# Kernel optimization log

Measured on AMD Instinct MI355X. Metric: run time of the kernel, lower is better.

## Reference

```python
import jax, jax.numpy as jnp
import numpy as np

MODES = 20
WIDTH = 64
EPS = 1e-5


def spectral_conv(x, w1, w2, m1, m2):
    # x: [B, C, H, W] real; w1, w2: [Ci, Co, m1, m2, 2] (real/imag)
    B, C, H, W = x.shape
    xf = jnp.fft.rfft2(x, norm='ortho')  # [B, C, H, W//2+1] complex
    w1c = w1[..., 0] + 1j * w1[..., 1]
    w2c = w2[..., 0] + 1j * w2[..., 1]
    m1 = min(m1, H)
    m2 = min(m2, W // 2 + 1)
    top = jnp.einsum('bixy,ioxy->boxy', xf[:, :, :m1, :m2], w1c[:, :, :m1, :m2])
    bot = jnp.einsum('bixy,ioxy->boxy', xf[:, :, -m1:, :m2], w2c[:, :, :m1, :m2])
    out = jnp.zeros((B, w1.shape[1], H, W // 2 + 1), dtype=xf.dtype)
    out = out.at[:, :, :m1, :m2].set(top)
    out = out.at[:, :, H - m1:, :m2].set(bot)
    return jnp.fft.irfft2(out, s=(H, W), norm='ortho')


def batchnorm2d(x, gamma, beta):
    # training-mode BN over (B, H, W) per channel; x: [B, C, H, W]
    mean = jnp.mean(x, axis=(0, 2, 3), keepdims=True)
    var = jnp.var(x, axis=(0, 2, 3), keepdims=True)
    xn = (x - mean) * jax.lax.rsqrt(var + EPS)
    return xn * gamma[None, :, None, None] + beta[None, :, None, None]


def setup_inputs() -> dict:
    key = jax.random.key(0)
    ks = jax.random.split(key, 12)
    B, H, W, Tin2 = 8, 256, 256, 12
    scale = 1.0 / (WIDTH * WIDTH)
    return {
        'x': jax.random.normal(ks[0], (B, H, W, Tin2), jnp.float32),
        'fc0_w': jax.random.normal(ks[1], (Tin2, WIDTH), jnp.float32) * 0.1,
        'fc0_b': jnp.zeros((WIDTH,), jnp.float32),
        'sw1': scale * jax.random.normal(ks[2], (4, WIDTH, WIDTH, MODES, MODES, 2), jnp.float32),
        'sw2': scale * jax.random.normal(ks[3], (4, WIDTH, WIDTH, MODES, MODES, 2), jnp.float32),
        'cw': jax.random.normal(ks[4], (4, WIDTH, WIDTH), jnp.float32) * 0.1,
        'cb': jnp.zeros((4, WIDTH), jnp.float32),
        'bng': jnp.ones((4, WIDTH), jnp.float32),
        'bnb': jnp.zeros((4, WIDTH), jnp.float32),
        'fc1_w': jax.random.normal(ks[5], (WIDTH, 128), jnp.float32) * 0.1,
        'fc1_b': jnp.zeros((128,), jnp.float32),
        'fc2_w': jax.random.normal(ks[6], (128, 1), jnp.float32) * 0.1,
        'fc2_b': jnp.zeros((1,), jnp.float32),
    }


def reference(x, fc0_w, fc0_b, sw1, sw2, cw, cb, bng, bnb, fc1_w, fc1_b, fc2_w, fc2_b):
    # lift: [B, H, W, Tin+2] -> [B, C, H, W]
    h = jnp.einsum('bhwt,tc->bhwc', x, fc0_w) + fc0_b
    h = jnp.transpose(h, (0, 3, 1, 2))
    for l in range(4):
        spec = spectral_conv(h, sw1[l], sw2[l], MODES, MODES)
        lin = jnp.einsum('bihw,oi->bohw', h, cw[l]) + cb[l][None, :, None, None]
        h = batchnorm2d(spec + lin, bng[l], bnb[l])
        if l < 3:
            h = jax.nn.relu(h)
    h = jnp.transpose(h, (0, 2, 3, 1))  # [B, H, W, C]
    h = jax.nn.relu(jnp.einsum('bhwc,cd->bhwd', h, fc1_w) + fc1_b)
    out = jnp.einsum('bhwd,de->bhwe', h, fc2_w) + fc2_b
    return out
```

## Files before the change

### kernel.cpp

```cpp
#include <hip/hip_runtime.h>
#include <hip/hip_bf16.h>


__device__ __forceinline__ void gll16(const float* gsrc, float* ldst) {
    __builtin_amdgcn_global_load_lds(
        (const __attribute__((address_space(1))) void*)gsrc,
        (__attribute__((address_space(3))) void*)ldst, 16, 0, 0);
}

__device__ __forceinline__ unsigned bfp(float x) {
    unsigned u = __float_as_uint(x);
    return (u + 0x7fffu + ((u >> 16) & 1u)) >> 16;
}

#define UNPK(U, B4) \
    B4.x = __uint_as_float((U).x << 16); B4.y = __uint_as_float((U).x & 0xffff0000u); \
    B4.z = __uint_as_float((U).y << 16); B4.w = __uint_as_float((U).y & 0xffff0000u);

__global__ __launch_bounds__(256) void init_k(const float* __restrict__ cw,
                                              float* __restrict__ costab, float* __restrict__ sintab,
                                              float* __restrict__ EAt, float* __restrict__ Tw,
                                              float* __restrict__ cwT, float* __restrict__ stats,
                                              unsigned* __restrict__ Twh) {
    int idx = blockIdx.x * 256 + threadIdx.x;
    const float PH = 6.28318530717958647692f / 256.f;
    if (idx < 256) {
        float s, c; sincosf(idx * PH, &s, &c);
        costab[idx] = c; sintab[idx] = s;
    } else if (idx < 256 + 10240) {
        int e = idx - 256;
        int n = e >> 8, w = e & 255, ky = n >> 1;
        int r = (ky * w) & 255;
        float s, c; sincosf(r * PH, &s, &c);
        EAt[e] = (n & 1) ? -s : c;
    } else if (idx < 256 + 20480) {
        int e = idx - 10496;
        int kp = e >> 8, w = e & 255;
        int ky = kp >> 1, p = kp & 1;
        int r = (ky * w) & 255;
        float s, c; sincosf(r * PH, &s, &c);
        float v;
        if (ky == 0) v = p ? 0.f : (1.f / 16.f);
        else         v = p ? (-2.f / 16.f) * s : (2.f / 16.f) * c;
        Tw[e] = v;
    } else if (idx < 256 + 20480 + 16384) {
        int e = idx - 20736;
        int l = e >> 12, r2 = e & 4095;
        int i = r2 >> 6, o = r2 & 63;
        cwT[e] = cw[(l << 12) + (o << 6) + i];
    } else if (idx < 256 + 20480 + 16384 + 2048) {
        stats[idx - 37120] = 0.f;
    } else if (idx < 256 + 20480 + 16384 + 2048 + 5120) {
        int e = idx - 39168;
        int kp = e >> 7, w2 = e & 127;
        int ky = kp >> 1, p = kp & 1;
        float v0, v1;
        {
            int w = w2 << 1;
            int r = (ky * w) & 255;
            float s, c; sincosf(r * PH, &s, &c);
            v0 = (ky == 0) ? (p ? 0.f : (1.f / 16.f))
                           : (p ? (-2.f / 16.f) * s : (2.f / 16.f) * c);
            r = (ky * (w + 1)) & 255;
            sincosf(r * PH, &s, &c);
            v1 = (ky == 0) ? (p ? 0.f : (1.f / 16.f))
                           : (p ? (-2.f / 16.f) * s : (2.f / 16.f) * c);
        }
        Twh[e] = bfp(v0) | (bfp(v1) << 16);
    }
}

__global__ __launch_bounds__(256) void wtrans_k(const float* __restrict__ sw1,
                                                const float* __restrict__ sw2,
                                                unsigned int* __restrict__ wt) {
    int gid = blockIdx.x * 4 + (threadIdx.x >> 6);
    int o = threadIdx.x & 63;
    int xyc = gid % 25;
    int i = (gid / 25) & 63;
    int t2 = gid / 1600;
    const float* src = ((t2 & 1) ? sw2 : sw1) + (t2 >> 1) * 3276800;
    const float* sp = src + ((i * 64 + o) * 400 + xyc * 16) * 2;
    unsigned int* dp = wt + (size_t)(t2 * 400 + xyc * 16) * 4096 + i * 64 + o;
#pragma unroll
    for (int j = 0; j < 16; ++j) {
        float re = sp[2 * j], im = sp[2 * j + 1];
        dp[(size_t)j * 4096] = bfp(re) | (bfp(im) << 16);
    }
}

__global__ __launch_bounds__(256) void fc0_k(const float* __restrict__ x,
                                             const float* __restrict__ w,
                                             const float* __restrict__ bias,
                                             float* __restrict__ outb) {
    __shared__ float ws[768];
    __shared__ float bs[64];
    int tid = threadIdx.x;
    for (int i = tid; i < 768; i += 256) ws[i] = w[i];
    if (tid < 64) bs[tid] = bias[tid];
    __syncthreads();
    int pix = blockIdx.x * 256 + tid;
    int b = pix >> 16, hw = pix & 65535;
    float xv[12];
#pragma unroll
    for (int t = 0; t < 12; ++t) xv[t] = x[pix * 12 + t];
    int base = (b << 22) + hw;
    for (int c = 0; c < 64; ++c) {
        float a = bs[c];
#pragma unroll
        for (int t = 0; t < 12; ++t) a += xv[t] * ws[t * 64 + c];
        outb[base + (c << 16)] = a;
    }
}

__global__ __launch_bounds__(128) void dftw_k(const float* __restrict__ X,
                                              const float* __restrict__ EAt,
                                              float* __restrict__ T,
                                              const float* __restrict__ statsl,
                                              const float* __restrict__ g,
                                              const float* __restrict__ bt,
                                              int fuse) {
    __shared__ __align__(16) float Xs[32 * 68];
    __shared__ __align__(16) float Est[40 * 32];
    int tid = threadIdx.x;
    int tm = tid >> 3, tn = tid & 7;
    int row0 = blockIdx.x << 6;
    float sc = 1.f, sh = 0.f;
    if (fuse) {
        int c = (row0 >> 8) & 63;
        float ssum = statsl[c] + statsl[128 + c] + statsl[256 + c] + statsl[384 + c];
        float ssq  = statsl[64 + c] + statsl[192 + c] + statsl[320 + c] + statsl[448 + c];
        float mean = ssum * (1.f / 524288.f);
        float var = ssq * (1.f / 524288.f) - mean * mean;
        sc = g[c] * rsqrtf(var + 1e-5f);
        sh = bt[c] - mean * sc;
    }
    float acc[4][5];
#pragma unroll
    for (int i = 0; i < 4; ++i)
#pragma unroll
        for (int j = 0; j < 5; ++j) acc[i][j] = 0.f;

#pragma unroll 1
    for (int kc = 0; kc < 256; kc += 32) {
        __syncthreads();
#pragma unroll
        for (int r = 0; r < 4; ++r) {
            int m = tm + (r << 4);
            float4 v = *(const float4*)&X[(row0 + m) * 256 + kc + (tn << 2)];
            if (fuse) {
                v.x = fmaxf(fmaf(v.x, sc, sh), 0.f);
                v.y = fmaxf(fmaf(v.y, sc, sh), 0.f);
                v.z = fmaxf(fmaf(v.z, sc, sh), 0.f);
                v.w = fmaxf(fmaf(v.w, sc, sh), 0.f);
            }
            int kb = tn << 2;
            Xs[(kb + 0) * 68 + m] = v.x;
            Xs[(kb + 1) * 68 + m] = v.y;
            Xs[(kb + 2) * 68 + m] = v.z;
            Xs[(kb + 3) * 68 + m] = v.w;
        }
        for (int i = tid; i < 1280; i += 128) Est[i] = EAt[((i >> 5) << 8) + kc + (i & 31)];
        __syncthreads();
#pragma unroll 1
        for (int k4 = 0; k4 < 8; ++k4) {
            float4 e0 = *(const float4*)&Est[(tn * 5 + 0) * 32 + (k4 << 2)];
            float4 e1 = *(const float4*)&Est[(tn * 5 + 1) * 32 + (k4 << 2)];
            float4 e2 = *(const float4*)&Est[(tn * 5 + 2) * 32 + (k4 << 2)];
            float4 e3 = *(const float4*)&Est[(tn * 5 + 3) * 32 + (k4 << 2)];
            float4 e4 = *(const float4*)&Est[(tn * 5 + 4) * 32 + (k4 << 2)];
#pragma unroll
            for (int c2 = 0; c2 < 4; ++c2) {
                float4 a = *(const float4*)&Xs[((k4 << 2) + c2) * 68 + (tm << 2)];
                float ev0 = ((const float*)&e0)[c2];
                float ev1 = ((const float*)&e1)[c2];
                float ev2 = ((const float*)&e2)[c2];
                float ev3 = ((const float*)&e3)[c2];
                float ev4 = ((const float*)&e4)[c2];
                acc[0][0] += a.x * ev0; acc[1][0] += a.y * ev0; acc[2][0] += a.z * ev0; acc[3][0] += a.w * ev0;
                acc[0][1] += a.x * ev1; acc[1][1] += a.y * ev1; acc[2][1] += a.z * ev1; acc[3][1] += a.w * ev1;
                acc[0][2] += a.x * ev2; acc[1][2] += a.y * ev2; acc[2][2] += a.z * ev2; acc[3][2] += a.w * ev2;
                acc[0][3] += a.x * ev3; acc[1][3] += a.y * ev3; acc[2][3] += a.z * ev3; acc[3][3] += a.w * ev3;
                acc[0][4] += a.x * ev4; acc[1][4] += a.y * ev4; acc[2][4] += a.z * ev4; acc[3][4] += a.w * ev4;
            }
        }
    }
#pragma unroll
    for (int i = 0; i < 4; ++i) {
        int row = row0 + (tm << 2) + i;
#pragma unroll
        for (int j = 0; j < 5; ++j) T[row * 40 + tn * 5 + j] = acc[i][j];
    }
}

__global__ __launch_bounds__(256) void dfth_k(const float* __restrict__ T,
                                              const float* __restrict__ ct, const float* __restrict__ st,
                                              float* __restrict__ XF) {
    __shared__ __align__(16) float Ts[10240];
    __shared__ float cts[256], sts[256];
    int tid = threadIdx.x;
    int bc = blockIdx.x;
    for (int i = tid; i < 10240; i += 256) Ts[i] = T[bc * 10240 + i];
    cts[tid] = ct[tid]; sts[tid] = st[tid];
    __syncthreads();
    if (tid < 200) {
        int kxi = tid / 5, kyg = tid % 5;
        int kxa = kxi < 20 ? kxi : kxi + 216;
        float ar0 = 0, ai0 = 0, ar1 = 0, ai1 = 0, ar2 = 0, ai2 = 0, ar3 = 0, ai3 = 0;
        int r = 0;
#pragma unroll 1
        for (int h = 0; h < 256; ++h) {
            float cc = cts[r], sv = sts[r];
            r = (r + kxa) & 255;
            float4 v0 = *(const float4*)&Ts[h * 40 + (kyg << 3)];
            float4 v1 = *(const float4*)&Ts[h * 40 + (kyg << 3) + 4];
            ar0 += v0.x * cc + v0.y * sv;  ai0 += v0.y * cc - v0.x * sv;
            ar1 += v0.z * cc + v0.w * sv;  ai1 += v0.w * cc - v0.z * sv;
            ar2 += v1.x * cc + v1.y * sv;  ai2 += v1.y * cc - v1.x * sv;
            ar3 += v1.z * cc + v1.w * sv;  ai3 += v1.w * cc - v1.z * sv;
        }
        int b = bc >> 6, c = bc & 63;
        const float s = 1.f / 256.f;
        int A = (b * 40 + kxi) * 20 + (kyg << 2);
        float2* O = (float2*)XF;
        O[(A + 0) * 64 + c] = make_float2(ar0 * s, ai0 * s);
        O[(A + 1) * 64 + c] = make_float2(ar1 * s, ai1 * s);
        O[(A + 2) * 64 + c] = make_float2(ar2 * s, ai2 * s);
        O[(A + 3) * 64 + c] = make_float2(ar3 * s, ai3 * s);
    }
}

__global__ __launch_bounds__(512) void eins_t_k(const float* __restrict__ XF,
                                                const unsigned int* __restrict__ wtl,
                                                float* __restrict__ YF) {
    __shared__ float xfs[1024];
    int tid = threadIdx.x;
    int x = blockIdx.x / 20, y = blockIdx.x % 20;
    for (int i = tid; i < 1024; i += 512) {
        int b = i >> 7, rr = i & 127;
        xfs[i] = XF[(b * 40 + x) * 2560 + y * 128 + rr];
    }
    __syncthreads();
    int b = tid >> 6, o = tid & 63;
    const unsigned int* wp = wtl + (size_t)(((x < 20 ? 0 : 400) + (x % 20) * 20 + y)) * 4096 + o;
    float ar = 0.f, ai = 0.f;
#pragma unroll 8
    for (int i = 0; i < 64; ++i) {
        unsigned int wv = wp[i << 6];
        float wr = __uint_as_float(wv << 16);
        float wi = __uint_as_float(wv & 0xffff0000u);
        float xr = xfs[(b << 7) + (i << 1)];
        float xi = xfs[(b << 7) + (i << 1) + 1];
        ar += xr * wr - xi * wi;
        ai += xr * wi + xi * wr;
    }
    ((float2*)YF)[((b * 40 + x) * 20 + y) * 64 + o] = make_float2(ar, ai);
}

__global__ __launch_bounds__(512) void eins_k(const float* __restrict__ XF,
                                              const float* __restrict__ w1, const float* __restrict__ w2,
                                              float* __restrict__ YF) {
    __shared__ float xfs[1024];
    int tid = threadIdx.x;
    int x = blockIdx.x / 20, y = blockIdx.x % 20;
    for (int i = tid; i < 1024; i += 512) {
        int b = i >> 7, rr = i & 127;
        xfs[i] = XF[(b * 40 + x) * 2560 + y * 128 + rr];
    }
    __syncthreads();
    int b = tid >> 6, o = tid & 63;
    const float* wp = (x < 20) ? (w1 + (x * 20 + y) * 2) : (w2 + ((x - 20) * 20 + y) * 2);
    float ar = 0.f, ai = 0.f;
#pragma unroll 8
    for (int i = 0; i < 64; ++i) {
        float2 wv = *(const float2*)&wp[(i * 64 + o) * 800];
        float xr = xfs[(b << 7) + (i << 1)];
        float xi = xfs[(b << 7) + (i << 1) + 1];
        ar += xr * wv.x - xi * wv.y;
        ai += xr * wv.y + xi * wv.x;
    }
    ((float2*)YF)[((b * 40 + x) * 20 + y) * 64 + o] = make_float2(ar, ai);
}

__global__ __launch_bounds__(256) void idfth_k(const float* __restrict__ YF,
                                               const float* __restrict__ ct, const float* __restrict__ st,
                                               float* __restrict__ Z) {
    __shared__ __align__(16) float yfs[1600];
    __shared__ float cts[256], sts[256];
    int tid = threadIdx.x;
    int bc = blockIdx.x;
    int b = bc >> 6, co = bc & 63;
    for (int i = tid; i < 800; i += 256) {
        int kx = i / 20, ky = i % 20;
        float2 v = ((const float2*)YF)[((b * 40 + kx) * 20 + ky) * 64 + co];
        yfs[kx * 40 + 2 * ky] = v.x;
        yfs[kx * 40 + 2 * ky + 1] = v.y;
    }
    cts[tid] = ct[tid]; sts[tid] = st[tid];
    __syncthreads();
    int h = tid;
    float accr[20], acci[20];
#pragma unroll
    for (int q = 0; q < 20; ++q) { accr[q] = 0.f; acci[q] = 0.f; }
#pragma unroll 1
    for (int kxi = 0; kxi < 40; ++kxi) {
        int kxa = kxi < 20 ? kxi : kxi + 216;
        int r = (kxa * h) & 255;
        float cc = cts[r], sv = sts[r];
#pragma unroll
        for (int q = 0; q < 10; ++q) {
            float4 v = *(const float4*)&yfs[kxi * 40 + (q << 2)];
            accr[2 * q]     += v.x * cc - v.y * sv;  acci[2 * q]     += v.x * sv + v.y * cc;
            accr[2 * q + 1] += v.z * cc - v.w * sv;  acci[2 * q + 1] += v.z * sv + v.w * cc;
        }
    }
    const float s = 1.f / 16.f;
    int base = (bc * 256 + h) * 40;
#pragma unroll
    for (int q = 0; q < 10; ++q) {
        float4 o4;
        o4.x = accr[2 * q] * s;     o4.y = acci[2 * q] * s;
        o4.z = accr[2 * q + 1] * s; o4.w = acci[2 * q + 1] * s;
        *(float4*)&Z[base + (q << 2)] = o4;
    }
}

#define FMA2(I, AV, J, B4) \
    acc[I][J].x += (AV) * B4.x; acc[I][J].y += (AV) * B4.y; \
    acc[I][J].z += (AV) * B4.z; acc[I][J].w += (AV) * B4.w;

#define FMA_COL(J, B4) \
    FMA2(0, a0.x, J, B4) FMA2(1, a0.y, J, B4) FMA2(2, a0.z, J, B4) FMA2(3, a0.w, J, B4) \
    FMA2(4, a1.x, J, B4) FMA2(5, a1.y, J, B4) FMA2(6, a1.z, J, B4) FMA2(7, a1.w, J, B4)

__global__ __launch_bounds__(256) void speclin_k(const float* __restrict__ hin,
                                                 const float* __restrict__ Z,
                                                 const float* __restrict__ cwTl,
                                                 const unsigned* __restrict__ Twh,
                                                 const float* __restrict__ cbl,
                                                 float* __restrict__ pre,
                                                 float* __restrict__ statsl,
                                                 const float* __restrict__ statsp,
                                                 const float* __restrict__ gp,
                                                 const float* __restrict__ btp,
                                                 int fuse) {
    __shared__ __align__(16) float AZ[104 * 64];
    __shared__ __align__(16) unsigned short BsH[2][2048];
    __shared__ float scs[64], shs[64];
    int tid = threadIdx.x;
    int bh = blockIdx.x;
    int b = bh >> 8, h = bh & 255;
    int to = tid >> 5, tw = tid & 31;
    int o0 = to << 3;

    if (tid < 64) {
        float s = 1.f, so = 0.f;
        if (fuse) {
            float ssum = statsp[tid] + statsp[128 + tid] + statsp[256 + tid] + statsp[384 + tid];
            float ssq  = statsp[64 + tid] + statsp[192 + tid] + statsp[320 + tid] + statsp[448 + tid];
            float mean = ssum * (1.f / 524288.f);
            float var = ssq * (1.f / 524288.f) - mean * mean;
            s = gp[tid] * rsqrtf(var + 1e-5f);
            so = btp[tid] - mean * s;
        }
        scs[tid] = s; shs[tid] = so;
    }
#pragma unroll
    for (int t = 0; t < 4; ++t) {
        int i4 = tid + (t << 8);
        gll16(&cwTl[i4 << 2], &AZ[i4 << 2]);
    }
    {
        const float* Zrow = Z + ((size_t)(((b << 6) << 8) + h)) * 40;
#pragma unroll
        for (int t = 0; t < 3; ++t) {
            int i4 = tid + (t << 8);
            if (i4 < 640) {
                int q = i4 % 10, o = i4 / 10;
                float4 v = *(const float4*)&Zrow[o * 10240 + (q << 2)];
                int rb = ((64 + (q << 2)) << 6) + o;
                AZ[rb] = v.x; AZ[rb + 64] = v.y; AZ[rb + 128] = v.z; AZ[rb + 192] = v.w;
            }
        }
    }
    const float* hrow = hin + ((size_t)(((b << 6) << 8) + h) << 8);
    float4 st[2];
#pragma unroll
    for (int t = 0; t < 2; ++t) {
        int i4 = tid + (t << 8);
        st[t] = *(const float4*)&hrow[((i4 >> 6) << 16) + ((i4 & 63) << 2)];
    }
    __syncthreads();
#pragma unroll
    for (int t = 0; t < 2; ++t) {
        int i4 = tid + (t << 8);
        int k = i4 >> 6, w4 = i4 & 63;
        float4 v = st[t];
        if (fuse) {
            float sck = scs[k], shk = shs[k];
            v.x = fmaxf(fmaf(v.x, sck, shk), 0.f);
            v.y = fmaxf(fmaf(v.y, sck, shk), 0.f);
            v.z = fmaxf(fmaf(v.z, sck, shk), 0.f);
            v.w = fmaxf(fmaf(v.w, sck, shk), 0.f);
        }
        uint2 u = make_uint2(bfp(v.x) | (bfp(v.y) << 16), bfp(v.z) | (bfp(v.w) << 16));
        *(uint2*)&BsH[0][(k << 8) + (w4 << 2)] = u;
    }
    __syncthreads();

    float4 acc[8][2];
#pragma unroll
    for (int i = 0; i < 8; ++i) {
        acc[i][0] = make_float4(0.f, 0.f, 0.f, 0.f);
        acc[i][1] = make_float4(0.f, 0.f, 0.f, 0.f);
    }

    int cur = 0;
    uint2 stw[2];
#pragma unroll 1
    for (int ch = 0; ch < 8; ++ch) {
        if (ch < 7) {
#pragma unroll
            for (int t = 0; t < 2; ++t) {
                int i4 = tid + (t << 8);
                st[t] = *(const float4*)&hrow[((((ch + 1) << 3) + (i4 >> 6)) << 16) + ((i4 & 63) << 2)];
            }
        } else {
#pragma unroll
            for (int t = 0; t < 2; ++t)
                stw[t] = *(const uint2*)&Twh[(t << 9) + (tid << 1)];
        }
        const unsigned short* Bc = BsH[cur];
        const float* Ac = &AZ[((ch << 3) << 6) + o0];
#pragma unroll 2
        for (int kk = 0; kk < 8; ++kk) {
            float4 a0 = *(const float4*)&Ac[(kk << 6)];
            float4 a1 = *(const float4*)&Ac[(kk << 6) + 4];
            uint2 u0 = *(const uint2*)&Bc[(kk << 8) + (tw << 2)];
            uint2 u1 = *(const uint2*)&Bc[(kk << 8) + 128 + (tw << 2)];
            float4 b0, b1;
            UNPK(u0, b0)
            UNPK(u1, b1)
            FMA_COL(0, b0)
            FMA_COL(1, b1)
        }
        if (ch < 7) {
#pragma unroll
            for (int t = 0; t < 2; ++t) {
                int i4 = tid + (t << 8);
                int k = i4 >> 6, w4 = i4 & 63;
                float4 v = st[t];
                if (fuse) {
                    float sck = scs[((ch + 1) << 3) + k], shk = shs[((ch + 1) << 3) + k];
                    v.x = fmaxf(fmaf(v.x, sck, shk), 0.f);
                    v.y = fmaxf(fmaf(v.y, sck, shk), 0.f);
                    v.z = fmaxf(fmaf(v.z, sck, shk), 0.f);
                    v.w = fmaxf(fmaf(v.w, sck, shk), 0.f);
                }
                uint2 u = make_uint2(bfp(v.x) | (bfp(v.y) << 16), bfp(v.z) | (bfp(v.w) << 16));
                *(uint2*)&BsH[cur ^ 1][(k << 8) + (w4 << 2)] = u;
            }
        } else {
#pragma unroll
            for (int t = 0; t < 2; ++t)
                *(uint2*)&BsH[cur ^ 1][(((t << 9) + (tid << 1)) << 1)] = stw[t];
        }
        __syncthreads();
        cur ^= 1;
    }

#pragma unroll 1
    for (int ch = 0; ch < 5; ++ch) {
        if (ch < 4) {
#pragma unroll
            for (int t = 0; t < 2; ++t)
                stw[t] = *(const uint2*)&Twh[((ch + 1) << 10) + (t << 9) + (tid << 1)];
        }
        const unsigned short* Bc = BsH[cur];
        const float* Ac = &AZ[(((ch << 3) + 64) << 6) + o0];
#pragma unroll 2
        for (int kk = 0; kk < 8; ++kk) {
            float4 a0 = *(const float4*)&Ac[(kk << 6)];
            float4 a1 = *(const float4*)&Ac[(kk << 6) + 4];
            uint2 u0 = *(const uint2*)&Bc[(kk << 8) + (tw << 2)];
            uint2 u1 = *(const uint2*)&Bc[(kk << 8) + 128 + (tw << 2)];
            float4 b0, b1;
            UNPK(u0, b0)
            UNPK(u1, b1)
            FMA_COL(0, b0)
            FMA_COL(1, b1)
        }
        if (ch < 4) {
#pragma unroll
            for (int t = 0; t < 2; ++t)
                *(uint2*)&BsH[cur ^ 1][(((t << 9) + (tid << 1)) << 1)] = stw[t];
        }
        __syncthreads();
        cur ^= 1;
    }

    float* srep = statsl + ((bh & 3) << 7);
#pragma unroll
    for (int i = 0; i < 8; ++i) {
        float cbv = cbl[o0 + i];
        float sum = 0.f, sq = 0.f;
        size_t obase = ((size_t)((((b << 6) + o0 + i) << 8) + h) << 8);
#pragma unroll
        for (int j = 0; j < 2; ++j) {
            float4 v = acc[i][j];
            v.x += cbv; v.y += cbv; v.z += cbv; v.w += cbv;
            *(float4*)&pre[obase + (j << 7) + (tw << 2)] = v;
            sum += v.x + v.y + v.z + v.w;
            sq  += v.x * v.x + v.y * v.y + v.z * v.z + v.w * v.w;
        }
        sum += __shfl_xor(sum, 1);  sq += __shfl_xor(sq, 1);
        sum += __shfl_xor(sum, 2);  sq += __shfl_xor(sq, 2);
        sum += __shfl_xor(sum, 4);  sq += __shfl_xor(sq, 4);
        sum += __shfl_xor(sum, 8);  sq += __shfl_xor(sq, 8);
        sum += __shfl_xor(sum, 16); sq += __shfl_xor(sq, 16);
        if ((tid & 31) == 0) {
            atomicAdd(&srep[o0 + i], sum);
            atomicAdd(&srep[64 + o0 + i], sq);
        }
    }
}

__global__ __launch_bounds__(256, 2) void fc12_k(const float* __restrict__ hin,
                                                 const float* __restrict__ statsl,
                                                 const float* __restrict__ g,
                                                 const float* __restrict__ bt,
                                                 const float* __restrict__ w1, const float* __restrict__ b1,
                                                 const float* __restrict__ w2, const float* __restrict__ b2,
                                                 float* __restrict__ out) {
    __shared__ __align__(16) float As[64 * 128];
    __shared__ __align__(16) float Bs[2][2048];
    __shared__ float scs[64], shs[64], bias2[128];
    __shared__ __align__(16) float red[4 * 256];
    int tid = threadIdx.x;
    int bh = blockIdx.x;
    int b = bh >> 8, h = bh & 255;
    int to = tid >> 4, tw = tid & 15;
    int d0 = to << 3;

    if (tid < 64) {
        float ssum = statsl[tid] + statsl[128 + tid] + statsl[256 + tid] + statsl[384 + tid];
        float ssq  = statsl[64 + tid] + statsl[192 + tid] + statsl[320 + tid] + statsl[448 + tid];
        float mean = ssum * (1.f / 524288.f);
        float var = ssq * (1.f / 524288.f) - mean * mean;
        float s = g[tid] * rsqrtf(var + 1e-5f);
        scs[tid] = s; shs[tid] = bt[tid] - mean * s;
    }
    __syncthreads();
    for (int i = tid; i < 8192; i += 256) As[i] = w1[i] * scs[i >> 7];
    if (tid < 128) {
        float a = b1[tid];
        for (int c = 0; c < 64; ++c) a += shs[c] * w1[c * 128 + tid];
        bias2[tid] = a;
    }
    const float* hrow = hin + ((size_t)(((b << 6) << 8) + h) << 8);
#pragma unroll
    for (int t = 0; t < 2; ++t) {
        int i4 = tid + (t << 8);
        gll16(&hrow[((i4 >> 6) << 16) + ((i4 & 63) << 2)], &Bs[0][i4 << 2]);
    }
    __syncthreads();

    float4 acc[8][4];
#pragma unroll
    for (int i = 0; i < 8; ++i)
#pragma unroll
        for (int j = 0; j < 4; ++j) acc[i][j] = make_float4(0.f, 0.f, 0.f, 0.f);

    int cur = 0;
#pragma unroll 1
    for (int ch = 0; ch < 8; ++ch) {
        if (ch < 7) {
#pragma unroll
            for (int t = 0; t < 2; ++t) {
                int i4 = tid + (t << 8);
                int k = i4 >> 6, w4 = (i4 & 63) << 2;
                gll16(&hrow[((((ch + 1) << 3) + k) << 16) + w4], &Bs[cur ^ 1][i4 << 2]);
            }
        }
        const float* Bc = Bs[cur];
#pragma unroll 2
        for (int kk = 0; kk < 8; ++kk) {
            int gk = (ch << 3) + kk;
            float4 a0 = *(const float4*)&As[(gk << 7) + d0];
            float4 a1 = *(const float4*)&As[(gk << 7) + d0 + 4];
            float4 b0 = *(const float4*)&Bc[(kk << 8) + (tw << 2)];
            float4 b1 = *(const float4*)&Bc[(kk << 8) + 64 + (tw << 2)];
            FMA_COL(0, b0)
            FMA_COL(1, b1)
            float4 b2 = *(const float4*)&Bc[(kk << 8) + 128 + (tw << 2)];
            float4 b3 = *(const float4*)&Bc[(kk << 8) + 192 + (tw << 2)];
            FMA_COL(2, b2)
            FMA_COL(3, b3)
        }
        __syncthreads();
        cur ^= 1;
    }

    float bb[8], wv[8];
#pragma unroll
    for (int i = 0; i < 8; ++i) { bb[i] = bias2[d0 + i]; wv[i] = w2[d0 + i]; }
    float4 p[4];
#pragma unroll
    for (int j = 0; j < 4; ++j) {
        float4 v = make_float4(0.f, 0.f, 0.f, 0.f);
#pragma unroll
        for (int i = 0; i < 8; ++i) {
            v.x += fmaxf(acc[i][j].x + bb[i], 0.f) * wv[i];
            v.y += fmaxf(acc[i][j].y + bb[i], 0.f) * wv[i];
            v.z += fmaxf(acc[i][j].z + bb[i], 0.f) * wv[i];
            v.w += fmaxf(acc[i][j].w + bb[i], 0.f) * wv[i];
        }
        v.x += __shfl_xor(v.x, 16); v.y += __shfl_xor(v.y, 16);
        v.z += __shfl_xor(v.z, 16); v.w += __shfl_xor(v.w, 16);
        v.x += __shfl_xor(v.x, 32); v.y += __shfl_xor(v.y, 32);
        v.z += __shfl_xor(v.z, 32); v.w += __shfl_xor(v.w, 32);
        p[j] = v;
    }
    int wave = tid >> 6;
    if ((tid & 63) < 16) {
#pragma unroll
        for (int j = 0; j < 4; ++j)
            *(float4*)&red[(wave << 8) + (j << 6) + (tw << 2)] = p[j];
    }
    __syncthreads();
    float s2 = b2[0] + red[tid] + red[256 + tid] + red[512 + tid] + red[768 + tid];
    out[(b * 256 + h) * 256 + tid] = s2;
}

extern "C" void kernel_launch(void* const* d_in, const int* in_sizes, int n_in,
                              void* d_out, int out_size, void* d_ws, size_t ws_size,
                              hipStream_t stream) {
    (void)in_sizes; (void)n_in; (void)out_size;
    const float* x     = (const float*)d_in[0];
    const float* fc0_w = (const float*)d_in[1];
    const float* fc0_b = (const float*)d_in[2];
    const float* sw1   = (const float*)d_in[3];
    const float* sw2   = (const float*)d_in[4];
    const float* cw    = (const float*)d_in[5];
    const float* cb    = (const float*)d_in[6];
    const float* bng   = (const float*)d_in[7];
    const float* bnb   = (const float*)d_in[8];
    const float* fc1_w = (const float*)d_in[9];
    const float* fc1_b = (const float*)d_in[10];
    const float* fc2_w = (const float*)d_in[11];
    const float* fc2_b = (const float*)d_in[12];
    float* out = (float*)d_out;

    float* ws = (float*)d_ws;
    float* hbuf   = ws;
    float* tz     = hbuf + 33554432;
    float* xf     = tz + 5242880;
    float* yf     = xf + 819200;
    float* costab = yf + 819200;
    float* sintab = costab + 256;
    float* EAt    = sintab + 256;
    float* Tw     = EAt + 10240;
    float* cwT    = Tw + 10240;
    float* stats  = cwT + 16384;
    unsigned* Twh = (unsigned*)(stats + 2048);
    unsigned* wt  = Twh + 5120;

    size_t base_floats = 40473600 + 2048 + 5120;
    int use_wt = (ws_size >= (base_floats + 13107200ull) * 4ull) ? 1 : 0;

    init_k<<<173, 256, 0, stream>>>(cw, costab, sintab, EAt, Tw, cwT, stats, Twh);
    if (use_wt) wtrans_k<<<3200, 256, 0, stream>>>(sw1, sw2, wt);
    fc0_k<<<2048, 256, 0, stream>>>(x, fc0_w, fc0_b, hbuf);

    for (int l = 0; l < 4; ++l) {
        if (l == 0)
            dftw_k<<<2048, 128, 0, stream>>>(hbuf, EAt, tz, stats, bng, bnb, 0);
        else
            dftw_k<<<2048, 128, 0, stream>>>(hbuf, EAt, tz, stats + (l - 1) * 512,
                                             bng + (l - 1) * 64, bnb + (l - 1) * 64, 1);
        dfth_k<<<512, 256, 0, stream>>>(tz, costab, sintab, xf);
        if (use_wt)
            eins_t_k<<<800, 512, 0, stream>>>(xf, wt + (size_t)l * 2 * 400 * 4096, yf);
        else
            eins_k<<<800, 512, 0, stream>>>(xf, sw1 + l * 3276800, sw2 + l * 3276800, yf);
        idfth_k<<<512, 256, 0, stream>>>(yf, costab, sintab, tz);
        speclin_k<<<2048, 256, 0, stream>>>(hbuf, tz, cwT + l * 4096, Twh, cb + l * 64,
                                            hbuf, stats + l * 512,
                                            (l == 0) ? stats : stats + (l - 1) * 512,
                                            bng + (l ? (l - 1) * 64 : 0),
                                            bnb + (l ? (l - 1) * 64 : 0),
                                            l ? 1 : 0);
    }
    fc12_k<<<2048, 256, 0, stream>>>(hbuf, stats + 3 * 512, bng + 3 * 64, bnb + 3 * 64,
                                     fc1_w, fc1_b, fc2_w, fc2_b, out);
}
```

Baseline: 1.312 ms.

## Move speclin GEMM to bf16 MFMA with hi/lo split weights

Measured after the change: 1.799 ms. 37.1% more time.

```diff
diff --git a/kernel.cpp b/kernel.cpp
--- a/kernel.cpp
+++ b/kernel.cpp
@@ -1,6 +1,9 @@
 #include <hip/hip_runtime.h>
 #include <hip/hip_bf16.h>
 
+
+typedef __attribute__((ext_vector_type(8))) short bfrag;
+typedef __attribute__((ext_vector_type(4))) float f32x4;
 
 __device__ __forceinline__ void gll16(const float* gsrc, float* ldst) {
     __builtin_amdgcn_global_load_lds(
@@ -12,61 +15,50 @@
     unsigned u = __float_as_uint(x);
     return (u + 0x7fffu + ((u >> 16) & 1u)) >> 16;
 }
-
-#define UNPK(U, B4) \
-    B4.x = __uint_as_float((U).x << 16); B4.y = __uint_as_float((U).x & 0xffff0000u); \
-    B4.z = __uint_as_float((U).y << 16); B4.w = __uint_as_float((U).y & 0xffff0000u);
+__device__ __forceinline__ float ubf(unsigned h) { return __uint_as_float(h << 16); }
 
 __global__ __launch_bounds__(256) void init_k(const float* __restrict__ cw,
                                               float* __restrict__ costab, float* __restrict__ sintab,
-                                              float* __restrict__ EAt, float* __restrict__ Tw,
-                                              float* __restrict__ cwT, float* __restrict__ stats,
-                                              unsigned* __restrict__ Twh) {
+                                              float* __restrict__ EAt, float* __restrict__ stats,
+                                              unsigned* __restrict__ Twp, unsigned* __restrict__ cwPk) {
     int idx = blockIdx.x * 256 + threadIdx.x;
     const float PH = 6.28318530717958647692f / 256.f;
     if (idx < 256) {
         float s, c; sincosf(idx * PH, &s, &c);
         costab[idx] = c; sintab[idx] = s;
-    } else if (idx < 256 + 10240) {
+    } else if (idx < 10496) {
         int e = idx - 256;
         int n = e >> 8, w = e & 255, ky = n >> 1;
         int r = (ky * w) & 255;
         float s, c; sincosf(r * PH, &s, &c);
         EAt[e] = (n & 1) ? -s : c;
-    } else if (idx < 256 + 20480) {
-        int e = idx - 10496;
-        int kp = e >> 8, w = e & 255;
-        int ky = kp >> 1, p = kp & 1;
-        int r = (ky * w) & 255;
+    } else if (idx < 12544) {
+        stats[idx - 10496] = 0.f;
+    } else if (idx < 17664) {
+        int e = idx - 12544;
+        int kpp = e >> 8, w = e & 255;
+        int r = (kpp * w) & 255;
         float s, c; sincosf(r * PH, &s, &c);
-        float v;
-        if (ky == 0) v = p ? 0.f : (1.f / 16.f);
-        else         v = p ? (-2.f / 16.f) * s : (2.f / 16.f) * c;
-        Tw[e] = v;
-    } else if (idx < 256 + 20480 + 16384) {
-        int e = idx - 20736;
-        int l = e >> 12, r2 = e & 4095;
-        int i = r2 >> 6, o = r2 & 63;
-        cwT[e] = cw[(l << 12) + (o << 6) + i];
-    } else if (idx < 256 + 20480 + 16384 + 2048) {
-        stats[idx - 37120] = 0.f;
-    } else if (idx < 256 + 20480 + 16384 + 2048 + 5120) {
-        int e = idx - 39168;
-        int kp = e >> 7, w2 = e & 127;
-        int ky = kp >> 1, p = kp & 1;
         float v0, v1;
-        {
-            int w = w2 << 1;
-            int r = (ky * w) & 255;
-            float s, c; sincosf(r * PH, &s, &c);
-            v0 = (ky == 0) ? (p ? 0.f : (1.f / 16.f))
-                           : (p ? (-2.f / 16.f) * s : (2.f / 16.f) * c);
-            r = (ky * (w + 1)) & 255;
-            sincosf(r * PH, &s, &c);
-            v1 = (ky == 0) ? (p ? 0.f : (1.f / 16.f))
-                           : (p ? (-2.f / 16.f) * s : (2.f / 16.f) * c);
-        }
-        Twh[e] = bfp(v0) | (bfp(v1) << 16);
+        if (kpp == 0) { v0 = 1.f / 16.f; v1 = 0.f; }
+        else          { v0 = (2.f / 16.f) * c; v1 = (-2.f / 16.f) * s; }
+        Twp[e] = bfp(v0) | (bfp(v1) << 16);
+    } else if (idx < 19712) {
+        int e = idx - 17664;
+        int l = e >> 9, s = (e >> 6) & 7, o = e & 63;
+        const float* sp = cw + (((l << 6) + o) << 6) + (s << 3);
+        unsigned hi[4], lo[4];
+#pragma unroll
+        for (int j = 0; j < 4; ++j) {
+            float a = sp[2 * j], b = sp[2 * j + 1];
+            unsigned ha = bfp(a), hb = bfp(b);
+            hi[j] = ha | (hb << 16);
+            lo[j] = bfp(a - ubf(ha)) | (bfp(b - ubf(hb)) << 16);
+        }
+        unsigned* dh = cwPk + ((((l << 1) + 0) * 8 + s) * 64 + o) * 4;
+        unsigned* dl = cwPk + ((((l << 1) + 1) * 8 + s) * 64 + o) * 4;
+#pragma unroll
+        for (int j = 0; j < 4; ++j) { dh[j] = hi[j]; dl[j] = lo[j]; }
     }
 }
 
@@ -324,18 +316,10 @@
     }
 }
 
-#define FMA2(I, AV, J, B4) \
-    acc[I][J].x += (AV) * B4.x; acc[I][J].y += (AV) * B4.y; \
-    acc[I][J].z += (AV) * B4.z; acc[I][J].w += (AV) * B4.w;
-
-#define FMA_COL(J, B4) \
-    FMA2(0, a0.x, J, B4) FMA2(1, a0.y, J, B4) FMA2(2, a0.z, J, B4) FMA2(3, a0.w, J, B4) \
-    FMA2(4, a1.x, J, B4) FMA2(5, a1.y, J, B4) FMA2(6, a1.z, J, B4) FMA2(7, a1.w, J, B4)
-
 __global__ __launch_bounds__(256) void speclin_k(const float* __restrict__ hin,
                                                  const float* __restrict__ Z,
-                                                 const float* __restrict__ cwTl,
-                                                 const unsigned* __restrict__ Twh,
+                                                 const unsigned* __restrict__ cwPkl,
+                                                 const unsigned* __restrict__ Twp,
                                                  const float* __restrict__ cbl,
                                                  float* __restrict__ pre,
                                                  float* __restrict__ statsl,
@@ -343,14 +327,15 @@
                                                  const float* __restrict__ gp,
                                                  const float* __restrict__ btp,
                                                  int fuse) {
-    __shared__ __align__(16) float AZ[104 * 64];
-    __shared__ __align__(16) unsigned short BsH[2][2048];
-    __shared__ float scs[64], shs[64];
+    __shared__ __align__(16) unsigned Ah[4096];
+    __shared__ __align__(16) unsigned Al[4096];
+    __shared__ __align__(16) unsigned B2[16640];
+    __shared__ float scs[64], shs[64], cbs[64];
     int tid = threadIdx.x;
     int bh = blockIdx.x;
     int b = bh >> 8, h = bh & 255;
-    int to = tid >> 5, tw = tid & 31;
-    int o0 = to << 3;
+    int lane = tid & 63, wv = tid >> 6;
+    int lg = lane >> 4, li = lane & 15;
 
     if (tid < 64) {
         float s = 1.f, so = 0.f;
@@ -363,166 +348,155 @@
             so = btp[tid] - mean * s;
         }
         scs[tid] = s; shs[tid] = so;
-    }
-#pragma unroll
-    for (int t = 0; t < 4; ++t) {
-        int i4 = tid + (t << 8);
-        gll16(&cwTl[i4 << 2], &AZ[i4 << 2]);
-    }
-    {
-        const float* Zrow = Z + ((size_t)(((b << 6) << 8) + h)) * 40;
-#pragma unroll
-        for (int t = 0; t < 3; ++t) {
-            int i4 = tid + (t << 8);
-            if (i4 < 640) {
-                int q = i4 % 10, o = i4 / 10;
-                float4 v = *(const float4*)&Zrow[o * 10240 + (q << 2)];
-                int rb = ((64 + (q << 2)) << 6) + o;
-                AZ[rb] = v.x; AZ[rb + 64] = v.y; AZ[rb + 128] = v.z; AZ[rb + 192] = v.w;
-            }
-        }
-    }
-    const float* hrow = hin + ((size_t)(((b << 6) << 8) + h) << 8);
-    float4 st[2];
+        cbs[tid] = cbl[tid];
+    }
 #pragma unroll
     for (int t = 0; t < 2; ++t) {
-        int i4 = tid + (t << 8);
-        st[t] = *(const float4*)&hrow[((i4 >> 6) << 16) + ((i4 & 63) << 2)];
-    }
-    __syncthreads();
-#pragma unroll
-    for (int t = 0; t < 2; ++t) {
-        int i4 = tid + (t << 8);
-        int k = i4 >> 6, w4 = i4 & 63;
-        float4 v = st[t];
+        int sl = tid + (t << 8);
+        gll16((const float*)(cwPkl + (sl << 2)), (float*)&Ah[sl << 2]);
+        gll16((const float*)(cwPkl + 2048 + (sl << 2)), (float*)&Al[sl << 2]);
+    }
+    for (int rr = wv; rr < 20; rr += 4) {
+        gll16((const float*)(Twp + (rr << 8) + (lane << 2)),
+              (float*)&B2[(32 + rr) * 260 + (lane << 2)]);
+    }
+#pragma unroll
+    for (int t = 0; t < 3; ++t) {
+        int u = tid + (t << 8);
+        int r = u >> 6, c4 = u & 63;
+        *(uint4*)&B2[(52 + r) * 260 + (c4 << 2)] = make_uint4(0, 0, 0, 0);
+    }
+    if (tid < 192) {
+        *(uint4*)&Ah[(832 + tid) << 2] = make_uint4(0, 0, 0, 0);
+        *(uint4*)&Al[(832 + tid) << 2] = make_uint4(0, 0, 0, 0);
+    }
+    if (tid < 128) {
+        int o = tid >> 1, s = tid & 1;
+        const float* zp = Z + ((size_t)(((b << 6) + o) * 256 + h)) * 40 + s * 20;
+#pragma unroll
+        for (int q = 0; q < 5; ++q) {
+            float4 v = *(const float4*)&zp[q << 2];
+            int qz = s * 5 + q;
+            int slot = 8 + (qz >> 1);
+            int off = ((slot << 6) + o) << 2;
+            int half = (qz & 1) << 1;
+            unsigned hx = bfp(v.x), hy = bfp(v.y), hz = bfp(v.z), hw = bfp(v.w);
+            *(uint2*)&Ah[off + half] = make_uint2(hx | (hy << 16), hz | (hw << 16));
+            unsigned lx = bfp(v.x - ubf(hx)), ly = bfp(v.y - ubf(hy));
+            unsigned lz = bfp(v.z - ubf(hz)), lw = bfp(v.w - ubf(hw));
+            *(uint2*)&Al[off + half] = make_uint2(lx | (ly << 16), lz | (lw << 16));
+        }
+    }
+    __syncthreads();
+
+#pragma unroll 2
+    for (int t = 0; t < 8; ++t) {
+        int u = tid + (t << 8);
+        int kp = u >> 6, wq = u & 63;
+        const float* p0 = hin + ((size_t)(((b << 6) + 2 * kp) * 256 + h) << 8) + (wq << 2);
+        float4 v0 = *(const float4*)p0;
+        float4 v1 = *(const float4*)(p0 + 65536);
         if (fuse) {
-            float sck = scs[k], shk = shs[k];
-            v.x = fmaxf(fmaf(v.x, sck, shk), 0.f);
-            v.y = fmaxf(fmaf(v.y, sck, shk), 0.f);
-            v.z = fmaxf(fmaf(v.z, sck, shk), 0.f);
-            v.w = fmaxf(fmaf(v.w, sck, shk), 0.f);
-        }
-        uint2 u = make_uint2(bfp(v.x) | (bfp(v.y) << 16), bfp(v.z) | (bfp(v.w) << 16));
-        *(uint2*)&BsH[0][(k << 8) + (w4 << 2)] = u;
-    }
-    __syncthreads();
-
-    float4 acc[8][2];
-#pragma unroll
-    for (int i = 0; i < 8; ++i) {
-        acc[i][0] = make_float4(0.f, 0.f, 0.f, 0.f);
-        acc[i][1] = make_float4(0.f, 0.f, 0.f, 0.f);
-    }
-
-    int cur = 0;
-    uint2 stw[2];
+            float s0 = scs[2 * kp], o0 = shs[2 * kp];
+            float s1 = scs[2 * kp + 1], o1 = shs[2 * kp + 1];
+            v0.x = fmaxf(fmaf(v0.x, s0, o0), 0.f); v0.y = fmaxf(fmaf(v0.y, s0, o0), 0.f);
+            v0.z = fmaxf(fmaf(v0.z, s0, o0), 0.f); v0.w = fmaxf(fmaf(v0.w, s0, o0), 0.f);
+            v1.x = fmaxf(fmaf(v1.x, s1, o1), 0.f); v1.y = fmaxf(fmaf(v1.y, s1, o1), 0.f);
+            v1.z = fmaxf(fmaf(v1.z, s1, o1), 0.f); v1.w = fmaxf(fmaf(v1.w, s1, o1), 0.f);
+        }
+        uint4 w;
+        w.x = bfp(v0.x) | (bfp(v1.x) << 16);
+        w.y = bfp(v0.y) | (bfp(v1.y) << 16);
+        w.z = bfp(v0.z) | (bfp(v1.z) << 16);
+        w.w = bfp(v0.w) | (bfp(v1.w) << 16);
+        *(uint4*)&B2[kp * 260 + (wq << 2)] = w;
+    }
+    __syncthreads();
+
+    f32x4 acc[4][4];
+#pragma unroll
+    for (int m = 0; m < 4; ++m)
+#pragma unroll
+        for (int n = 0; n < 4; ++n) acc[m][n] = (f32x4){0.f, 0.f, 0.f, 0.f};
+
+    union UB { uint4 u; bfrag f; };
 #pragma unroll 1
-    for (int ch = 0; ch < 8; ++ch) {
-        if (ch < 7) {
-#pragma unroll
-            for (int t = 0; t < 2; ++t) {
-                int i4 = tid + (t << 8);
-                st[t] = *(const float4*)&hrow[((((ch + 1) << 3) + (i4 >> 6)) << 16) + ((i4 & 63) << 2)];
-            }
-        } else {
-#pragma unroll
-            for (int t = 0; t < 2; ++t)
-                stw[t] = *(const uint2*)&Twh[(t << 9) + (tid << 1)];
-        }
-        const unsigned short* Bc = BsH[cur];
-        const float* Ac = &AZ[((ch << 3) << 6) + o0];
-#pragma unroll 2
-        for (int kk = 0; kk < 8; ++kk) {
-            float4 a0 = *(const float4*)&Ac[(kk << 6)];
-            float4 a1 = *(const float4*)&Ac[(kk << 6) + 4];
-            uint2 u0 = *(const uint2*)&Bc[(kk << 8) + (tw << 2)];
-            uint2 u1 = *(const uint2*)&Bc[(kk << 8) + 128 + (tw << 2)];
-            float4 b0, b1;
-            UNPK(u0, b0)
-            UNPK(u1, b1)
-            FMA_COL(0, b0)
-            FMA_COL(1, b1)
-        }
-        if (ch < 7) {
-#pragma unroll
-            for (int t = 0; t < 2; ++t) {
-                int i4 = tid + (t << 8);
-                int k = i4 >> 6, w4 = i4 & 63;
-                float4 v = st[t];
-                if (fuse) {
-                    float sck = scs[((ch + 1) << 3) + k], shk = shs[((ch + 1) << 3) + k];
-                    v.x = fmaxf(fmaf(v.x, sck, shk), 0.f);
-                    v.y = fmaxf(fmaf(v.y, sck, shk), 0.f);
-                    v.z = fmaxf(fmaf(v.z, sck, shk), 0.f);
-                    v.w = fmaxf(fmaf(v.w, sck, shk), 0.f);
-                }
-                uint2 u = make_uint2(bfp(v.x) | (bfp(v.y) << 16), bfp(v.z) | (bfp(v.w) << 16));
-                *(uint2*)&BsH[cur ^ 1][(k << 8) + (w4 << 2)] = u;
-            }
-        } else {
-#pragma unroll
-            for (int t = 0; t < 2; ++t)
-                *(uint2*)&BsH[cur ^ 1][(((t << 9) + (tid << 1)) << 1)] = stw[t];
-        }
-        __syncthreads();
-        cur ^= 1;
-    }
-
-#pragma unroll 1
-    for (int ch = 0; ch < 5; ++ch) {
-        if (ch < 4) {
-#pragma unroll
-            for (int t = 0; t < 2; ++t)
-                stw[t] = *(const uint2*)&Twh[((ch + 1) << 10) + (t << 9) + (tid << 1)];
-        }
-        const unsigned short* Bc = BsH[cur];
-        const float* Ac = &AZ[(((ch << 3) + 64) << 6) + o0];
-#pragma unroll 2
-        for (int kk = 0; kk < 8; ++kk) {
-            float4 a0 = *(const float4*)&Ac[(kk << 6)];
-            float4 a1 = *(const float4*)&Ac[(kk << 6) + 4];
-            uint2 u0 = *(const uint2*)&Bc[(kk << 8) + (tw << 2)];
-            uint2 u1 = *(const uint2*)&Bc[(kk << 8) + 128 + (tw << 2)];
-            float4 b0, b1;
-            UNPK(u0, b0)
-            UNPK(u1, b1)
-            FMA_COL(0, b0)
-            FMA_COL(1, b1)
-        }
-        if (ch < 4) {
-#pragma unroll
-            for (int t = 0; t < 2; ++t)
-                *(uint2*)&BsH[cur ^ 1][(((t << 9) + (tid << 1)) << 1)] = stw[t];
-        }
-        __syncthreads();
-        cur ^= 1;
+    for (int kc = 0; kc < 4; ++kc) {
+        bfrag ah[4], al[4];
+#pragma unroll
+        for (int m = 0; m < 4; ++m) {
+            int sidx = (((kc << 2) + lg) << 6) + (m << 4) + li;
+            ah[m] = *(const bfrag*)&Ah[sidx << 2];
+            al[m] = *(const bfrag*)&Al[sidx << 2];
+        }
+        bfrag bfv[4];
+#pragma unroll
+        for (int n = 0; n < 4; ++n) {
+            int rbase = ((kc << 4) + (lg << 2)) * 260 + (wv << 6) + (n << 4) + li;
+            UB ub;
+            ub.u.x = B2[rbase];
+            ub.u.y = B2[rbase + 260];
+            ub.u.z = B2[rbase + 520];
+            ub.u.w = B2[rbase + 780];
+            bfv[n] = ub.f;
+        }
+#pragma unroll
+        for (int n = 0; n < 4; ++n)
+#pragma unroll
+            for (int m = 0; m < 4; ++m)
+                acc[m][n] = __builtin_amdgcn_mfma_f32_16x16x32_bf16(ah[m], bfv[n], acc[m][n], 0, 0, 0);
+#pragma unroll
+        for (int n = 0; n < 4; ++n)
+#pragma unroll
+            for (int m = 0; m < 4; ++m)
+                acc[m][n] = __builtin_amdgcn_mfma_f32_16x16x32_bf16(al[m], bfv[n], acc[m][n], 0, 0, 0);
     }
 
     float* srep = statsl + ((bh & 3) << 7);
 #pragma unroll
-    for (int i = 0; i < 8; ++i) {
-        float cbv = cbl[o0 + i];
-        float sum = 0.f, sq = 0.f;
-        size_t obase = ((size_t)((((b << 6) + o0 + i) << 8) + h) << 8);
-#pragma unroll
-        for (int j = 0; j < 2; ++j) {
-            float4 v = acc[i][j];
-            v.x += cbv; v.y += cbv; v.z += cbv; v.w += cbv;
-            *(float4*)&pre[obase + (j << 7) + (tw << 2)] = v;
-            sum += v.x + v.y + v.z + v.w;
-            sq  += v.x * v.x + v.y * v.y + v.z * v.z + v.w * v.w;
-        }
-        sum += __shfl_xor(sum, 1);  sq += __shfl_xor(sq, 1);
-        sum += __shfl_xor(sum, 2);  sq += __shfl_xor(sq, 2);
-        sum += __shfl_xor(sum, 4);  sq += __shfl_xor(sq, 4);
-        sum += __shfl_xor(sum, 8);  sq += __shfl_xor(sq, 8);
-        sum += __shfl_xor(sum, 16); sq += __shfl_xor(sq, 16);
-        if ((tid & 31) == 0) {
-            atomicAdd(&srep[o0 + i], sum);
-            atomicAdd(&srep[64 + o0 + i], sq);
-        }
-    }
-}
+    for (int m = 0; m < 4; ++m) {
+        int ob = (m << 4) + (lg << 2);
+        float4 cb4 = *(const float4*)&cbs[ob];
+        float sx = 0.f, sy = 0.f, sz = 0.f, sw = 0.f;
+        float qx = 0.f, qy = 0.f, qz = 0.f, qw = 0.f;
+#pragma unroll
+        for (int n = 0; n < 4; ++n) {
+            float vx = acc[m][n].x + cb4.x;
+            float vy = acc[m][n].y + cb4.y;
+            float vz = acc[m][n].z + cb4.z;
+            float vw = acc[m][n].w + cb4.w;
+            int wc = (wv << 6) + (n << 4) + li;
+            size_t base = ((size_t)(((b << 6) + ob) * 256 + h) << 8) + wc;
+            pre[base] = vx;
+            pre[base + 65536] = vy;
+            pre[base + 131072] = vz;
+            pre[base + 196608] = vw;
+            sx += vx; sy += vy; sz += vz; sw += vw;
+            qx += vx * vx; qy += vy * vy; qz += vz * vz; qw += vw * vw;
+        }
+#pragma unroll
+        for (int msk = 1; msk < 16; msk <<= 1) {
+            sx += __shfl_xor(sx, msk); sy += __shfl_xor(sy, msk);
+            sz += __shfl_xor(sz, msk); sw += __shfl_xor(sw, msk);
+            qx += __shfl_xor(qx, msk); qy += __shfl_xor(qy, msk);
+            qz += __shfl_xor(qz, msk); qw += __shfl_xor(qw, msk);
+        }
+        if (li == 0) {
+            atomicAdd(&srep[ob + 0], sx); atomicAdd(&srep[ob + 1], sy);
+            atomicAdd(&srep[ob + 2], sz); atomicAdd(&srep[ob + 3], sw);
+            atomicAdd(&srep[64 + ob + 0], qx); atomicAdd(&srep[64 + ob + 1], qy);
+            atomicAdd(&srep[64 + ob + 2], qz); atomicAdd(&srep[64 + ob + 3], qw);
+        }
+    }
+}
+
+#define FMA2(I, AV, J, B4) \
+    acc[I][J].x += (AV) * B4.x; acc[I][J].y += (AV) * B4.y; \
+    acc[I][J].z += (AV) * B4.z; acc[I][J].w += (AV) * B4.w;
+
+#define FMA_COL(J, B4) \
+    FMA2(0, a0.x, J, B4) FMA2(1, a0.y, J, B4) FMA2(2, a0.z, J, B4) FMA2(3, a0.w, J, B4) \
+    FMA2(4, a1.x, J, B4) FMA2(5, a1.y, J, B4) FMA2(6, a1.z, J, B4) FMA2(7, a1.w, J, B4)
 
 __global__ __launch_bounds__(256, 2) void fc12_k(const float* __restrict__ hin,
                                                  const float* __restrict__ statsl,
@@ -658,16 +632,15 @@
     float* costab = yf + 819200;
     float* sintab = costab + 256;
     float* EAt    = sintab + 256;
-    float* Tw     = EAt + 10240;
-    float* cwT    = Tw + 10240;
-    float* stats  = cwT + 16384;
-    unsigned* Twh = (unsigned*)(stats + 2048);
-    unsigned* wt  = Twh + 5120;
-
-    size_t base_floats = 40473600 + 2048 + 5120;
+    float* stats  = EAt + 10240;
+    unsigned* Twp  = (unsigned*)(stats + 2048);
+    unsigned* cwPk = Twp + 5120;
+    unsigned* wt   = cwPk + 16384;
+
+    size_t base_floats = 40470016;
     int use_wt = (ws_size >= (base_floats + 13107200ull) * 4ull) ? 1 : 0;
 
-    init_k<<<173, 256, 0, stream>>>(cw, costab, sintab, EAt, Tw, cwT, stats, Twh);
+    init_k<<<77, 256, 0, stream>>>(cw, costab, sintab, EAt, stats, Twp, cwPk);
     if (use_wt) wtrans_k<<<3200, 256, 0, stream>>>(sw1, sw2, wt);
     fc0_k<<<2048, 256, 0, stream>>>(x, fc0_w, fc0_b, hbuf);
 
@@ -683,7 +656,7 @@
         else
             eins_k<<<800, 512, 0, stream>>>(xf, sw1 + l * 3276800, sw2 + l * 3276800, yf);
         idfth_k<<<512, 256, 0, stream>>>(yf, costab, sintab, tz);
-        speclin_k<<<2048, 256, 0, stream>>>(hbuf, tz, cwT + l * 4096, Twh, cb + l * 64,
+        speclin_k<<<2048, 256, 0, stream>>>(hbuf, tz, cwPk + l * 4096, Twp, cb + l * 64,
                                             hbuf, stats + l * 512,
                                             (l == 0) ? stats : stats + (l - 1) * 512,
                                             bng + (l ? (l - 1) * 64 : 0),
```
